# Kernel tuning notes

Measured on AMD Instinct MI355X. Metric: run time of the kernel, lower is better.

The kernel has to match this reference:

```python
import jax, jax.numpy as jnp
import numpy as np

DOWNSCALE = 2


def avg_pool2d(x, s):
    b, c, h, w = x.shape
    return x.reshape(b, c, h // s, s, w // s, s).mean(axis=(3, 5))


def upsample_bilinear_align_corners(x, s):
    # matches torch nn.Upsample(scale_factor=s, mode='bilinear', align_corners=True)
    b, c, h, w = x.shape
    H, W = h * s, w * s
    ys = jnp.arange(H, dtype=x.dtype) * ((h - 1) / (H - 1))
    xs = jnp.arange(W, dtype=x.dtype) * ((w - 1) / (W - 1))
    y0 = jnp.floor(ys).astype(jnp.int32)
    y1 = jnp.minimum(y0 + 1, h - 1)
    wy = (ys - y0.astype(x.dtype))[None, None, :, None]
    x0 = jnp.floor(xs).astype(jnp.int32)
    x1 = jnp.minimum(x0 + 1, w - 1)
    wx = (xs - x0.astype(x.dtype))[None, None, None, :]
    rows = x[:, :, y0, :] * (1 - wy) + x[:, :, y1, :] * wy  # [b,c,H,w]
    return rows[:, :, :, x0] * (1 - wx) + rows[:, :, :, x1] * wx  # [b,c,H,W]


def setup_inputs() -> dict:
    key = jax.random.key(0)
    k1, k2, k3, k4, k5, k6 = jax.random.split(key, 6)
    B, INCH, MIDCH, H, W = 8, 64, 32, 128, 128
    primary = jax.random.normal(k1, (B, INCH, H, W), dtype=jnp.float32)
    cross = jax.random.normal(k2, (B, INCH, H, W), dtype=jnp.float32)
    w_theta = jax.random.normal(k3, (MIDCH, INCH), dtype=jnp.float32) / np.sqrt(INCH)
    w_phi = jax.random.normal(k4, (MIDCH, INCH), dtype=jnp.float32) / np.sqrt(INCH)
    w_g = jax.random.normal(k5, (MIDCH, INCH), dtype=jnp.float32) / np.sqrt(INCH)
    w_out = jax.random.normal(k6, (INCH, MIDCH, 3, 3), dtype=jnp.float32) / np.sqrt(MIDCH * 9)
    return {"primary": primary, "cross": cross, "w_theta": w_theta,
            "w_phi": w_phi, "w_g": w_g, "w_out": w_out}


def reference(primary, cross, w_theta, w_phi, w_g, w_out):
    pd = avg_pool2d(primary, DOWNSCALE)  # [b,c,h,w]
    cd = avg_pool2d(cross, DOWNSCALE)
    b, c, h, w = pd.shape
    n = h * w
    pd_flat = pd.reshape(b, c, n)
    cd_flat = cd.reshape(b, c, n)
    # 1x1 convs -> matmuls over channel dim
    g = jnp.einsum('mc,bcn->bnm', w_g, pd_flat)       # [b,n,mid]
    theta = jnp.einsum('mc,bcn->bnm', w_theta, cd_flat)  # queries from cross
    phi = jnp.einsum('mc,bcn->bmn', w_phi, pd_flat)      # keys from primary
    attn = jax.nn.softmax(jnp.einsum('bnm,bmk->bnk', theta, phi), axis=-1)  # [b,n,n]
    y = jnp.einsum('bnk,bkm->bmn', attn, g).reshape(b, -1, h, w)  # [b,mid,h,w]
    y = upsample_bilinear_align_corners(y, DOWNSCALE)
    out = jax.lax.conv_general_dilated(
        y, w_out, window_strides=(1, 1), padding='SAME',
        dimension_numbers=('NCHW', 'OIHW', 'NCHW'))
    return jnp.concatenate((primary, out), axis=1)
```

## Files before the change

### kernel.cpp

```cpp
#include <hip/hip_runtime.h>
#include <math.h>

typedef _Float16 f16;
typedef f16 f16x8 __attribute__((ext_vector_type(8)));
typedef f16 f16x4 __attribute__((ext_vector_type(4)));
typedef __fp16 fp16x2 __attribute__((ext_vector_type(2)));
typedef float f32x4 __attribute__((ext_vector_type(4)));

#define LOG2E 1.44269504088896340736f

__global__ __launch_bounds__(256) void prep_kernel(
    const float* __restrict__ w, const float* __restrict__ w_theta,
    const float* __restrict__ w_phi, const float* __restrict__ w_g,
    f16* __restrict__ wT, float* __restrict__ wTr)
{
    int id = blockIdx.x * 256 + threadIdx.x;
    if (id < 18432) {
        int oc = id / 288, k = id % 288;
        int tap = k >> 5, c = k & 31;
        wT[id] = (f16)w[((size_t)oc * 32 + c) * 9 + tap];
    } else {
        int t2 = id - 18432;
        int tensor = t2 >> 11, idx = t2 & 2047;
        int c = idx >> 5, m = idx & 31;
        const float* src = tensor == 0 ? w_theta : (tensor == 1 ? w_phi : w_g);
        wTr[tensor * 2048 + c * 32 + m] = src[m * 64 + c];
    }
}

__global__ __launch_bounds__(256) void pool_project_kernel(
    const float* __restrict__ primary, const float* __restrict__ cross,
    const float* __restrict__ wTr,
    f16* __restrict__ theta, f16* __restrict__ phi, f16* __restrict__ gP,
    float* __restrict__ out)
{
    __shared__ __align__(16) float pool[2 * 1024];
    __shared__ __align__(16) float wls[3 * 2048];
    int t = threadIdx.x;
    int bx = blockIdx.x;
    int b = bx >> 8, rem = bx & 255;
    int row = rem >> 2, q4 = rem & 3;

#pragma unroll
    for (int i = 0; i < 4; ++i) {
        int chunk = i * 256 + t;
        int xq = chunk & 7;
        int c = (chunk >> 3) & 63, ts = chunk >> 9;
        const float* src = ts ? cross : primary;
        const float* rp = src + (size_t)b * 1048576 + (size_t)c * 16384
                        + (size_t)(2 * row) * 128 + q4 * 32 + xq * 4;
        float4 v0 = *(const float4*)rp;
        float4 v1 = *(const float4*)(rp + 128);
        if (ts == 0) {
            float* ob = out + ((size_t)b * 128 + c) * 16384
                      + (size_t)(2 * row) * 128 + q4 * 32 + xq * 4;
            *(float4*)ob = v0;
            *(float4*)(ob + 128) = v1;
        }
        float2 pv;
        pv.x = 0.25f * ((v0.x + v0.y) + (v1.x + v1.y));
        pv.y = 0.25f * ((v0.z + v0.w) + (v1.z + v1.w));
        *(float2*)&pool[ts * 1024 + c * 16 + 2 * xq] = pv;
    }
#pragma unroll
    for (int i = 0; i < 6; ++i) {
        int cw = i * 256 + t;
        *(float4*)&wls[cw * 4] = *(const float4*)(wTr + cw * 4);
    }
    __syncthreads();

    int mg = t >> 6, lane = t & 63;
    int cg = lane >> 4, px = lane & 15;

    const float* pbaseL = pool + (cg * 16) * 16 + px;
    const float* cbaseL = pbaseL + 1024;
    const float* wlt = wls + (cg * 16) * 32 + mg * 8;
    const float* wlp = wlt + 2048;
    const float* wlg = wlt + 4096;

    float th[8], ph[8], gg[8];
#pragma unroll
    for (int j = 0; j < 8; ++j) { th[j] = 0.f; ph[j] = 0.f; gg[j] = 0.f; }

#pragma unroll
    for (int ci = 0; ci < 16; ++ci) {
        float pdc = pbaseL[ci * 16];
        float cdc = cbaseL[ci * 16];
        float4 a0 = *(const float4*)(wlt + ci * 32);
        float4 a1 = *(const float4*)(wlt + ci * 32 + 4);
        float4 b0 = *(const float4*)(wlp + ci * 32);
        float4 b1 = *(const float4*)(wlp + ci * 32 + 4);
        float4 g0 = *(const float4*)(wlg + ci * 32);
        float4 g1 = *(const float4*)(wlg + ci * 32 + 4);
        th[0] = fmaf(a0.x, cdc, th[0]); th[1] = fmaf(a0.y, cdc, th[1]);
        th[2] = fmaf(a0.z, cdc, th[2]); th[3] = fmaf(a0.w, cdc, th[3]);
        th[4] = fmaf(a1.x, cdc, th[4]); th[5] = fmaf(a1.y, cdc, th[5]);
        th[6] = fmaf(a1.z, cdc, th[6]); th[7] = fmaf(a1.w, cdc, th[7]);
        ph[0] = fmaf(b0.x, pdc, ph[0]); ph[1] = fmaf(b0.y, pdc, ph[1]);
        ph[2] = fmaf(b0.z, pdc, ph[2]); ph[3] = fmaf(b0.w, pdc, ph[3]);
        ph[4] = fmaf(b1.x, pdc, ph[4]); ph[5] = fmaf(b1.y, pdc, ph[5]);
        ph[6] = fmaf(b1.z, pdc, ph[6]); ph[7] = fmaf(b1.w, pdc, ph[7]);
        gg[0] = fmaf(g0.x, pdc, gg[0]); gg[1] = fmaf(g0.y, pdc, gg[1]);
        gg[2] = fmaf(g0.z, pdc, gg[2]); gg[3] = fmaf(g0.w, pdc, gg[3]);
        gg[4] = fmaf(g1.x, pdc, gg[4]); gg[5] = fmaf(g1.y, pdc, gg[5]);
        gg[6] = fmaf(g1.z, pdc, gg[6]); gg[7] = fmaf(g1.w, pdc, gg[7]);
    }

#pragma unroll
    for (int j = 0; j < 8; ++j) {
        th[j] += __shfl_xor(th[j], 16); th[j] += __shfl_xor(th[j], 32);
        ph[j] += __shfl_xor(ph[j], 16); ph[j] += __shfl_xor(ph[j], 32);
        gg[j] += __shfl_xor(gg[j], 16); gg[j] += __shfl_xor(gg[j], 32);
    }

    int n = row * 64 + q4 * 16 + px;
    if (cg == 0) {
        f16x8 tv;
#pragma unroll
        for (int j = 0; j < 8; ++j) tv[j] = (f16)(th[j] * LOG2E);
        *(f16x8*)(theta + ((size_t)b * 4096 + n) * 32 + mg * 8) = tv;
    } else if (cg == 1) {
        f16x8 pv;
#pragma unroll
        for (int j = 0; j < 8; ++j) pv[j] = (f16)ph[j];
        *(f16x8*)(phi + ((size_t)b * 4096 + n) * 32 + mg * 8) = pv;
    } else {
        int w = n & 31, nb32 = n & ~31;
        int d = ((w >> 2) & 3) * 8 + (w >> 4) * 4 + (w & 3);
        int jbase = (cg - 2) * 4;
#pragma unroll
        for (int jj = 0; jj < 4; ++jj) {
            int m = mg * 8 + jbase + jj;
            gP[((size_t)b * 32 + m) * 4096 + nb32 + d] = (f16)gg[jbase + jj];
        }
    }
}

__global__ __launch_bounds__(256) void attn_kernel(
    const f16* __restrict__ theta, const f16* __restrict__ phi,
    const f16* __restrict__ gP, f16* __restrict__ ypart,
    float* __restrict__ lpart)
{
    __shared__ __align__(16) f16 phiS[2][128 * 40];
    __shared__ __align__(16) f16 gS[2][32 * 136];
    int t = threadIdx.x;
    int wid = t >> 6, lane = t & 63;
    int g = lane >> 4, c15 = lane & 15;
    int b = blockIdx.y, sp = blockIdx.z;
    int qb = blockIdx.x * 128 + wid * 32;

    f16x8 a_thA = *(const f16x8*)(theta + ((size_t)b * 4096 + qb + c15) * 32 + g * 8);
    f16x8 a_thB = *(const f16x8*)(theta + ((size_t)b * 4096 + qb + 16 + c15) * 32 + g * 8);

    f32x4 YA0 = {0.f, 0.f, 0.f, 0.f}, YA1 = {0.f, 0.f, 0.f, 0.f};
    f32x4 YB0 = {0.f, 0.f, 0.f, 0.f}, YB1 = {0.f, 0.f, 0.f, 0.f};
    float lsumA = 0.f, lsumB = 0.f;
    const f32x4 zinit = {-12.f, -12.f, -12.f, -12.f};

    const f16* phiB = phi + (size_t)b * 4096 * 32;
    const f16* gB   = gP  + (size_t)b * 32 * 4096;

    int i1 = t, i2 = t + 256;
    int odp1 = (i1 >> 2) * 40 + (i1 & 3) * 8;
    int odp2 = (i2 >> 2) * 40 + (i2 & 3) * 8;
    int odg1 = (i1 >> 4) * 136 + (i1 & 15) * 8;
    int odg2 = (i2 >> 4) * 136 + (i2 & 15) * 8;
    const f16* sp1 = phiB + (size_t)(i1 >> 2) * 32 + (i1 & 3) * 8;
    const f16* sp2 = phiB + (size_t)(i2 >> 2) * 32 + (i2 & 3) * 8;
    const f16* sg1 = gB + (size_t)(i1 >> 4) * 4096 + (i1 & 15) * 8;
    const f16* sg2 = gB + (size_t)(i2 >> 4) * 4096 + (i2 & 15) * 8;

    const int ktbeg = sp * 8, ktend = sp * 8 + 8;

    uint4 r0 = *(const uint4*)(sp1 + (size_t)(ktbeg * 128) * 32);
    uint4 r1 = *(const uint4*)(sp2 + (size_t)(ktbeg * 128) * 32);
    uint4 r2 = *(const uint4*)(sg1 + ktbeg * 128);
    uint4 r3 = *(const uint4*)(sg2 + ktbeg * 128);

    int cur = 0;
    for (int kt = ktbeg; kt < ktend; ++kt) {
        *(uint4*)&phiS[cur][odp1] = r0;
        *(uint4*)&phiS[cur][odp2] = r1;
        *(uint4*)&gS[cur][odg1] = r2;
        *(uint4*)&gS[cur][odg2] = r3;
        if (kt + 1 < ktend) {
            int n1 = (kt + 1) * 128;
            r0 = *(const uint4*)(sp1 + (size_t)n1 * 32);
            r1 = *(const uint4*)(sp2 + (size_t)n1 * 32);
            r2 = *(const uint4*)(sg1 + n1);
            r3 = *(const uint4*)(sg2 + n1);
        }
        __syncthreads();

        const f16* pS = phiS[cur];
        const f16* gSS = gS[cur];
#pragma unroll
        for (int u = 0; u < 4; ++u) {
            f16x8 bf0 = *(const f16x8*)(pS + (2 * u * 16 + c15) * 40 + g * 8);
            f16x8 bf1 = *(const f16x8*)(pS + ((2 * u + 1) * 16 + c15) * 40 + g * 8);
            f16x8 ga0 = *(const f16x8*)(gSS + c15 * 136 + u * 32 + g * 8);
            f16x8 ga1 = *(const f16x8*)(gSS + (16 + c15) * 136 + u * 32 + g * 8);

            f32x4 s0A = __builtin_amdgcn_mfma_f32_16x16x32_f16(bf0, a_thA, zinit, 0, 0, 0);
            f32x4 s1A = __builtin_amdgcn_mfma_f32_16x16x32_f16(bf1, a_thA, zinit, 0, 0, 0);
            f32x4 s0B = __builtin_amdgcn_mfma_f32_16x16x32_f16(bf0, a_thB, zinit, 0, 0, 0);
            f32x4 s1B = __builtin_amdgcn_mfma_f32_16x16x32_f16(bf1, a_thB, zinit, 0, 0, 0);

            union { unsigned int u4[4]; f16x8 v; } pbA, pbB;
#pragma unroll
            for (int half = 0; half < 2; ++half) {
                f32x4 sv = half ? s1A : s0A;
                float p0 = __builtin_amdgcn_exp2f(sv[0]);
                float p1 = __builtin_amdgcn_exp2f(sv[1]);
                float p2 = __builtin_amdgcn_exp2f(sv[2]);
                float p3 = __builtin_amdgcn_exp2f(sv[3]);
                lsumA += (p0 + p1) + (p2 + p3);
                union { fp16x2 v; unsigned int u; } ca, cb;
                ca.v = __builtin_amdgcn_cvt_pkrtz(p0, p1);
                cb.v = __builtin_amdgcn_cvt_pkrtz(p2, p3);
                pbA.u4[half * 2 + 0] = ca.u;
                pbA.u4[half * 2 + 1] = cb.u;
            }
#pragma unroll
            for (int half = 0; half < 2; ++half) {
                f32x4 sv = half ? s1B : s0B;
                float p0 = __builtin_amdgcn_exp2f(sv[0]);
                float p1 = __builtin_amdgcn_exp2f(sv[1]);
                float p2 = __builtin_amdgcn_exp2f(sv[2]);
                float p3 = __builtin_amdgcn_exp2f(sv[3]);
                lsumB += (p0 + p1) + (p2 + p3);
                union { fp16x2 v; unsigned int u; } ca, cb;
                ca.v = __builtin_amdgcn_cvt_pkrtz(p0, p1);
                cb.v = __builtin_amdgcn_cvt_pkrtz(p2, p3);
                pbB.u4[half * 2 + 0] = ca.u;
                pbB.u4[half * 2 + 1] = cb.u;
            }
            YA0 = __builtin_amdgcn_mfma_f32_16x16x32_f16(ga0, pbA.v, YA0, 0, 0, 0);
            YA1 = __builtin_amdgcn_mfma_f32_16x16x32_f16(ga1, pbA.v, YA1, 0, 0, 0);
            YB0 = __builtin_amdgcn_mfma_f32_16x16x32_f16(ga0, pbB.v, YB0, 0, 0, 0);
            YB1 = __builtin_amdgcn_mfma_f32_16x16x32_f16(ga1, pbB.v, YB1, 0, 0, 0);
        }
        cur ^= 1;
    }

    lsumA += __shfl_xor(lsumA, 16);
    lsumA += __shfl_xor(lsumA, 32);
    lsumB += __shfl_xor(lsumB, 16);
    lsumB += __shfl_xor(lsumB, 32);
    if (g == 0) {
        lpart[((size_t)(sp * 8 + b)) * 4096 + qb + c15] = lsumA;
        lpart[((size_t)(sp * 8 + b)) * 4096 + qb + 16 + c15] = lsumB;
    }

    f16* yp = ypart + ((size_t)(sp * 8 + b) * 32) * 4096 + qb;
#pragma unroll
    for (int r = 0; r < 4; ++r) {
        yp[(size_t)(g * 4 + r) * 4096 + c15]           = (f16)YA0[r];
        yp[(size_t)(16 + g * 4 + r) * 4096 + c15]      = (f16)YA1[r];
        yp[(size_t)(g * 4 + r) * 4096 + 16 + c15]      = (f16)YB0[r];
        yp[(size_t)(16 + g * 4 + r) * 4096 + 16 + c15] = (f16)YB1[r];
    }
}

__global__ __launch_bounds__(256) void combine_kernel(
    const f16* __restrict__ ypart, const float* __restrict__ lpart,
    float* __restrict__ y)
{
    int gid = blockIdx.x * 256 + threadIdx.x;
    int n4 = (gid & 1023) * 4;
    int bm = gid >> 10;
    int b = bm >> 5, m = bm & 31;
    float acc0 = 0.f, acc1 = 0.f, acc2 = 0.f, acc3 = 0.f;
    float l0 = 0.f, l1 = 0.f, l2 = 0.f, l3 = 0.f;
#pragma unroll
    for (int s = 0; s < 4; ++s) {
        f16x4 yv = *(const f16x4*)(ypart + ((size_t)(s * 8 + b) * 32 + m) * 4096 + n4);
        float4 lv = *(const float4*)(lpart + ((size_t)(s * 8 + b)) * 4096 + n4);
        acc0 += (float)yv[0]; acc1 += (float)yv[1];
        acc2 += (float)yv[2]; acc3 += (float)yv[3];
        l0 += lv.x; l1 += lv.y; l2 += lv.z; l3 += lv.w;
    }
    float4 o = make_float4(acc0 / l0, acc1 / l1, acc2 / l2, acc3 / l3);
    *(float4*)(y + (size_t)bm * 4096 + n4) = o;
}

__global__ __launch_bounds__(256) void upsample_kernel(
    const float* __restrict__ y, f16* __restrict__ yup)
{
    int gid = blockIdx.x * 256 + threadIdx.x;
    int xi = gid & 63, Y = (gid >> 6) & 127, bc = gid >> 13;
    const float r = 63.0f / 127.0f;
    float fy = (float)Y * r;
    int y0 = (int)fy; int y1 = min(y0 + 1, 63);
    float wy = fy - (float)y0;
    const float* r0 = y + (size_t)bc * 4096 + y0 * 64;
    const float* r1 = y + (size_t)bc * 4096 + y1 * 64;
    union { unsigned int u; f16 h[2]; } pk;
#pragma unroll
    for (int k = 0; k < 2; ++k) {
        int X = 2 * xi + k;
        float fx = (float)X * r;
        int x0 = (int)fx; int x1 = min(x0 + 1, 63);
        float wx = fx - (float)x0;
        float a  = r0[x0] * (1.f - wy) + r1[x0] * wy;
        float bb = r0[x1] * (1.f - wy) + r1[x1] * wy;
        pk.h[k] = (f16)(a * (1.f - wx) + bb * wx);
    }
    *(unsigned int*)&yup[((size_t)bc * 128 + Y) * 128 + 2 * xi] = pk.u;
}

__global__ __launch_bounds__(256) void conv3x3_kernel(
    const f16* __restrict__ yup, const f16* __restrict__ wT,
    float* __restrict__ out)
{
    __shared__ f16 tile[32 * 4 * 132];
    int tY = blockIdx.x, b = blockIdx.y;
    int t = threadIdx.x;

    {
        int u = t & 127, c = u >> 2, rr = u & 3;
        int s0 = c * 528 + rr * 132 + ((t < 128) ? 0 : 130);
        *(unsigned int*)&tile[s0] = 0u;
    }
#pragma unroll
    for (int rd = 0; rd < 8; ++rd) {
        int id = rd * 256 + t;
        int c = id >> 6, rr = (id >> 4) & 3, seg = id & 15;
        int iy = 2 * tY - 1 + rr;
        uint4 v = make_uint4(0u, 0u, 0u, 0u);
        if ((unsigned)iy < 128u)
            v = *(const uint4*)(yup + (((size_t)b * 32 + c) * 128 + iy) * 128 + seg * 8);
        int base = c * 528 + rr * 132 + 2 + seg * 8;
        *(unsigned int*)&tile[base + 0] = v.x;
        *(unsigned int*)&tile[base + 2] = v.y;
        *(unsigned int*)&tile[base + 4] = v.z;
        *(unsigned int*)&tile[base + 6] = v.w;
    }
    __syncthreads();

    int wid = t >> 6, lane = t & 63, g = lane >> 4, c15 = lane & 15;
    f32x4 acc[4][4];
#pragma unroll
    for (int mt = 0; mt < 4; ++mt)
#pragma unroll
        for (int nt = 0; nt < 4; ++nt) acc[mt][nt] = (f32x4){0.f, 0.f, 0.f, 0.f};

#pragma unroll
    for (int tap = 0; tap < 9; ++tap) {
        const int dy = tap / 3, dx = tap % 3;
        f16x8 a0 = *(const f16x8*)(wT + (size_t)(c15) * 288 + tap * 32 + g * 8);
        f16x8 a1 = *(const f16x8*)(wT + (size_t)(16 + c15) * 288 + tap * 32 + g * 8);
        f16x8 a2 = *(const f16x8*)(wT + (size_t)(32 + c15) * 288 + tap * 32 + g * 8);
        f16x8 a3 = *(const f16x8*)(wT + (size_t)(48 + c15) * 288 + tap * 32 + g * 8);
#pragma unroll
        for (int nt = 0; nt < 4; ++nt) {
            int ntg = wid * 4 + nt;
            int r_out = ntg >> 3, x0 = (ntg & 7) * 16;
            int base = (g * 8) * 528 + (r_out + dy) * 132 + 1 + x0 + c15 + dx;
            f16x8 bf;
#pragma unroll
            for (int j = 0; j < 8; ++j) bf[j] = tile[base + j * 528];
            acc[0][nt] = __builtin_amdgcn_mfma_f32_16x16x32_f16(a0, bf, acc[0][nt], 0, 0, 0);
            acc[1][nt] = __builtin_amdgcn_mfma_f32_16x16x32_f16(a1, bf, acc[1][nt], 0, 0, 0);
            acc[2][nt] = __builtin_amdgcn_mfma_f32_16x16x32_f16(a2, bf, acc[2][nt], 0, 0, 0);
            acc[3][nt] = __builtin_amdgcn_mfma_f32_16x16x32_f16(a3, bf, acc[3][nt], 0, 0, 0);
        }
    }

#pragma unroll
    for (int mt = 0; mt < 4; ++mt)
#pragma unroll
        for (int nt = 0; nt < 4; ++nt) {
            int ntg = wid * 4 + nt;
            int r_out = ntg >> 3, x0 = (ntg & 7) * 16;
            float* ob = out + ((size_t)b * 128 + 64 + mt * 16 + g * 4) * 16384
                            + (2 * tY + r_out) * 128 + x0 + c15;
#pragma unroll
            for (int r = 0; r < 4; ++r)
                ob[(size_t)r * 16384] = acc[mt][nt][r];
        }
}

extern "C" void kernel_launch(void* const* d_in, const int* in_sizes, int n_in,
                              void* d_out, int out_size, void* d_ws, size_t ws_size,
                              hipStream_t stream)
{
    const float* primary = (const float*)d_in[0];
    const float* cross   = (const float*)d_in[1];
    const float* w_theta = (const float*)d_in[2];
    const float* w_phi   = (const float*)d_in[3];
    const float* w_g     = (const float*)d_in[4];
    const float* w_out   = (const float*)d_in[5];
    float* out = (float*)d_out;

    char* wsb = (char*)d_ws;
    f16*   wT    = (f16*)(wsb);
    float* wTr   = (float*)(wsb + 36864);
    f16*   theta = (f16*)(wsb + (1u << 16));
    f16*   phi   = (f16*)(wsb + (1u << 16) + (2u << 20));
    f16*   gP    = (f16*)(wsb + (1u << 16) + (4u << 20));
    float* y     = (float*)(wsb + (1u << 16) + (6u << 20));
    f16*   yup   = (f16*)(wsb + (1u << 16) + (10u << 20));
    f16*   ypart = (f16*)(wsb + (1u << 16) + (18u << 20));
    float* lpart = (float*)(wsb + (1u << 16) + (26u << 20));

    prep_kernel<<<96, 256, 0, stream>>>(w_out, w_theta, w_phi, w_g, wT, wTr);
    pool_project_kernel<<<2048, 256, 0, stream>>>(primary, cross, wTr,
                                                  theta, phi, gP, out);
    attn_kernel<<<dim3(32, 8, 4), 256, 0, stream>>>(theta, phi, gP, ypart, lpart);
    combine_kernel<<<1024, 256, 0, stream>>>(ypart, lpart, y);
    upsample_kernel<<<8192, 256, 0, stream>>>(y, yup);
    conv3x3_kernel<<<dim3(64, 8), 256, 0, stream>>>(yup, wT, out);
}
```

Measured before the change: 84.58 us.

## Fuse split-K combine and bilinear upsample into conv3x3 tile loader

The separate combine and upsample kernels are removed. The conv kernel now sums the four split partial outputs and their normalizers for the few low-res rows its tile needs, stages them in shared memory, and interpolates directly into the f16 conv tile. This drops two launches and the global round trips through the y and yup buffers. In exchange each conv block recomputes overlapping low-res rows, uses more shared memory, and has a longer serial prologue before the MFMA loop.

Measured after the change: 95.22 us. 1.13x slower.

```diff
diff --git a/kernel.cpp b/kernel.cpp
--- a/kernel.cpp
+++ b/kernel.cpp
@@ -262,79 +262,94 @@
     }
 }
 
-__global__ __launch_bounds__(256) void combine_kernel(
+__global__ __launch_bounds__(256) void conv3x3_kernel(
     const f16* __restrict__ ypart, const float* __restrict__ lpart,
-    float* __restrict__ y)
+    const f16* __restrict__ wT, float* __restrict__ out)
 {
-    int gid = blockIdx.x * 256 + threadIdx.x;
-    int n4 = (gid & 1023) * 4;
-    int bm = gid >> 10;
-    int b = bm >> 5, m = bm & 31;
-    float acc0 = 0.f, acc1 = 0.f, acc2 = 0.f, acc3 = 0.f;
-    float l0 = 0.f, l1 = 0.f, l2 = 0.f, l3 = 0.f;
-#pragma unroll
-    for (int s = 0; s < 4; ++s) {
-        f16x4 yv = *(const f16x4*)(ypart + ((size_t)(s * 8 + b) * 32 + m) * 4096 + n4);
-        float4 lv = *(const float4*)(lpart + ((size_t)(s * 8 + b)) * 4096 + n4);
-        acc0 += (float)yv[0]; acc1 += (float)yv[1];
-        acc2 += (float)yv[2]; acc3 += (float)yv[3];
-        l0 += lv.x; l1 += lv.y; l2 += lv.z; l3 += lv.w;
-    }
-    float4 o = make_float4(acc0 / l0, acc1 / l1, acc2 / l2, acc3 / l3);
-    *(float4*)(y + (size_t)bm * 4096 + n4) = o;
-}
-
-__global__ __launch_bounds__(256) void upsample_kernel(
-    const float* __restrict__ y, f16* __restrict__ yup)
-{
-    int gid = blockIdx.x * 256 + threadIdx.x;
-    int xi = gid & 63, Y = (gid >> 6) & 127, bc = gid >> 13;
-    const float r = 63.0f / 127.0f;
-    float fy = (float)Y * r;
-    int y0 = (int)fy; int y1 = min(y0 + 1, 63);
-    float wy = fy - (float)y0;
-    const float* r0 = y + (size_t)bc * 4096 + y0 * 64;
-    const float* r1 = y + (size_t)bc * 4096 + y1 * 64;
-    union { unsigned int u; f16 h[2]; } pk;
-#pragma unroll
-    for (int k = 0; k < 2; ++k) {
-        int X = 2 * xi + k;
-        float fx = (float)X * r;
-        int x0 = (int)fx; int x1 = min(x0 + 1, 63);
-        float wx = fx - (float)x0;
-        float a  = r0[x0] * (1.f - wy) + r1[x0] * wy;
-        float bb = r0[x1] * (1.f - wy) + r1[x1] * wy;
-        pk.h[k] = (f16)(a * (1.f - wx) + bb * wx);
-    }
-    *(unsigned int*)&yup[((size_t)bc * 128 + Y) * 128 + 2 * xi] = pk.u;
-}
-
-__global__ __launch_bounds__(256) void conv3x3_kernel(
-    const f16* __restrict__ yup, const f16* __restrict__ wT,
-    float* __restrict__ out)
-{
+    __shared__ float ybuf[32][4][66];
+    __shared__ float linv[4][64];
+    __shared__ float wxt[128];
+    __shared__ int   x1t[128];
     __shared__ f16 tile[32 * 4 * 132];
     int tY = blockIdx.x, b = blockIdx.y;
     int t = threadIdx.x;
 
+    int num = (2 * tY - 1) * 63;
+    int ylo = num >= 0 ? (num / 127) : 0;
+    if (ylo > 60) ylo = 60;
+
+    if (t < 128) {
+        float fx = (float)t * (63.0f / 127.0f);
+        int x0 = (int)fx;
+        wxt[t] = fx - (float)x0;
+        x1t[t] = x0;
+    }
     {
-        int u = t & 127, c = u >> 2, rr = u & 3;
-        int s0 = c * 528 + rr * 132 + ((t < 128) ? 0 : 130);
+        int rr = t >> 6, xx = t & 63;
+        float l = 0.f;
+#pragma unroll
+        for (int s = 0; s < 4; ++s)
+            l += lpart[((size_t)(s * 8 + b)) * 4096 + (ylo + rr) * 64 + xx];
+        linv[rr][xx] = 1.0f / l;
+    }
+    {
+        int u = t & 127, c = u >> 2, rr2 = u & 3;
+        int s0 = c * 528 + rr2 * 132 + ((t < 128) ? 0 : 130);
         *(unsigned int*)&tile[s0] = 0u;
     }
-#pragma unroll
-    for (int rd = 0; rd < 8; ++rd) {
-        int id = rd * 256 + t;
-        int c = id >> 6, rr = (id >> 4) & 3, seg = id & 15;
-        int iy = 2 * tY - 1 + rr;
-        uint4 v = make_uint4(0u, 0u, 0u, 0u);
-        if ((unsigned)iy < 128u)
-            v = *(const uint4*)(yup + (((size_t)b * 32 + c) * 128 + iy) * 128 + seg * 8);
-        int base = c * 528 + rr * 132 + 2 + seg * 8;
-        *(unsigned int*)&tile[base + 0] = v.x;
-        *(unsigned int*)&tile[base + 2] = v.y;
-        *(unsigned int*)&tile[base + 4] = v.z;
-        *(unsigned int*)&tile[base + 6] = v.w;
+    __syncthreads();
+
+    {
+        int m = t >> 3, q = t & 7;
+#pragma unroll
+        for (int rr = 0; rr < 4; ++rr) {
+            float acc[8];
+#pragma unroll
+            for (int j = 0; j < 8; ++j) acc[j] = 0.f;
+#pragma unroll
+            for (int s = 0; s < 4; ++s) {
+                f16x8 v = *(const f16x8*)(ypart
+                    + ((size_t)(s * 8 + b) * 32 + m) * 4096 + (ylo + rr) * 64 + q * 8);
+#pragma unroll
+                for (int j = 0; j < 8; ++j) acc[j] += (float)v[j];
+            }
+#pragma unroll
+            for (int j = 0; j < 8; ++j)
+                ybuf[m][rr][q * 8 + j] = acc[j] * linv[rr][q * 8 + j];
+        }
+    }
+    __syncthreads();
+
+    {
+        const float r = 63.0f / 127.0f;
+        int c = t >> 3, xs = (t & 7) * 16;
+#pragma unroll
+        for (int rr = 0; rr < 4; ++rr) {
+            int Y = 2 * tY - 1 + rr;
+            bool ok = (unsigned)Y < 128u;
+            float fy = ok ? (float)Y * r : 0.f;
+            int y0 = (int)fy;
+            int y1 = min(y0 + 1, 63);
+            float wy = fy - (float)y0;
+            int r0i = ok ? (y0 - ylo) : 0;
+            int r1i = ok ? (y1 - ylo) : 0;
+            const float* row0 = ybuf[c][r0i];
+            const float* row1 = ybuf[c][r1i];
+#pragma unroll
+            for (int j = 0; j < 16; ++j) {
+                int X = xs + j;
+                f16 val = (f16)0.f;
+                if (ok) {
+                    int x0 = x1t[X];
+                    int x1 = min(x0 + 1, 63);
+                    float wx = wxt[X];
+                    float a  = row0[x0] * (1.f - wx) + row0[x1] * wx;
+                    float bb = row1[x0] * (1.f - wx) + row1[x1] * wx;
+                    val = (f16)(a * (1.f - wy) + bb * wy);
+                }
+                tile[c * 528 + rr * 132 + 2 + X] = val;
+            }
+        }
     }
     __syncthreads();
 
@@ -399,8 +414,6 @@
     f16*   theta = (f16*)(wsb + (1u << 16));
     f16*   phi   = (f16*)(wsb + (1u << 16) + (2u << 20));
     f16*   gP    = (f16*)(wsb + (1u << 16) + (4u << 20));
-    float* y     = (float*)(wsb + (1u << 16) + (6u << 20));
-    f16*   yup   = (f16*)(wsb + (1u << 16) + (10u << 20));
     f16*   ypart = (f16*)(wsb + (1u << 16) + (18u << 20));
     float* lpart = (float*)(wsb + (1u << 16) + (26u << 20));
 
@@ -408,7 +421,5 @@
     pool_project_kernel<<<2048, 256, 0, stream>>>(primary, cross, wTr,
                                                   theta, phi, gP, out);
     attn_kernel<<<dim3(32, 8, 4), 256, 0, stream>>>(theta, phi, gP, ypart, lpart);
-    combine_kernel<<<1024, 256, 0, stream>>>(ypart, lpart, y);
-    upsample_kernel<<<8192, 256, 0, stream>>>(y, yup);
-    conv3x3_kernel<<<dim3(64, 8), 256, 0, stream>>>(yup, wT, out);
+    conv3x3_kernel<<<dim3(64, 8), 256, 0, stream>>>(ypart, lpart, wT, out);
 }
```
